# Kernel tuning notes

Measured on AMD Instinct MI355X. Metric: run time of the kernel, lower is better.

## Reference

```python
import jax, jax.numpy as jnp
import numpy as np

EMBED, HEADS, LEVELS, POINTS = 256, 8, 4, 4
HD = EMBED // HEADS
BS, NQ = 2, 16384
SHAPES = [(128, 128), (64, 64), (32, 32), (16, 16)]  # (H, W) per level
NV = sum(h * w for h, w in SHAPES)
EPS = 1e-5


def layernorm(x, g, b):
    mu = jnp.mean(x, -1, keepdims=True)
    var = jnp.mean((x - mu) ** 2, -1, keepdims=True)
    return (x - mu) / jnp.sqrt(var + EPS) * g + b


def bilinear_sample(vl, loc, H, W):
    # vl: (bs, heads, H*W, hd); loc: (bs, nq, heads, P, 2) normalized [0,1]
    # grid_sample semantics: align_corners=False, zero padding
    x = loc[..., 0] * W - 0.5
    y = loc[..., 1] * H - 0.5
    x0 = jnp.floor(x)
    y0 = jnp.floor(y)
    lx, ly = x - x0, y - y0
    x0 = x0.astype(jnp.int32)
    y0 = y0.astype(jnp.int32)
    gather = jax.vmap(jax.vmap(lambda t, i: t[i]))  # over (bs, heads)
    acc = None
    for dx, dy, w in ((0, 0, (1 - lx) * (1 - ly)), (1, 0, lx * (1 - ly)),
                      (0, 1, (1 - lx) * ly), (1, 1, lx * ly)):
        xi, yi = x0 + dx, y0 + dy
        valid = ((xi >= 0) & (xi < W) & (yi >= 0) & (yi < H)).astype(vl.dtype)
        idx = jnp.clip(yi, 0, H - 1) * W + jnp.clip(xi, 0, W - 1)
        idx = idx.transpose(0, 2, 1, 3)           # (bs, heads, nq, P)
        g = gather(vl, idx)                       # (bs, heads, nq, P, hd)
        wv = (w * valid).transpose(0, 2, 1, 3)[..., None]
        acc = g * wv if acc is None else acc + g * wv
    return acc


def forward(lidar_feat, feat_flatten, ref_2d, spatial_shapes, level_start_index,
            q_pose, W_off, b_off, W_attn, b_attn, W_val, b_val, W_out, b_out,
            ln1_g, ln1_b, ffn_w1, ffn_w2, ln2_g, ln2_b):
    identity = lidar_feat                         # (nq, bs, C)
    q = (lidar_feat + q_pose).transpose(1, 0, 2)  # (bs, nq, C)
    bs, nq, C = q.shape
    v = feat_flatten.transpose(1, 0, 2) @ W_val + b_val
    v = v.reshape(bs, -1, HEADS, HD)
    off = (q @ W_off + b_off).reshape(bs, nq, HEADS, LEVELS, POINTS, 2)
    aw = (q @ W_attn + b_attn).reshape(bs, nq, HEADS, LEVELS * POINTS)
    aw = jax.nn.softmax(aw, -1).reshape(bs, nq, HEADS, LEVELS, POINTS)
    ss = np.asarray(spatial_shapes)               # static level shapes
    lsi = np.asarray(level_start_index)
    norm = jnp.asarray(ss[:, ::-1].copy(), q.dtype)  # (L, 2) [W, H]
    loc = ref_2d[:, :, None, :, None, :] + off / norm[None, None, None, :, None, :]
    out = jnp.zeros((bs, nq, HEADS, HD), q.dtype)
    for l in range(LEVELS):
        H, W = int(ss[l, 0]), int(ss[l, 1])
        s = int(lsi[l])
        vl = v[:, s:s + H * W].transpose(0, 2, 1, 3)   # (bs, heads, HW, hd)
        sampled = bilinear_sample(vl, loc[:, :, :, l], H, W)
        out = out + jnp.einsum('bhqpd,bqhp->bqhd', sampled, aw[:, :, :, l, :])
    out = out.reshape(bs, nq, C) @ W_out + b_out
    out = out.transpose(1, 0, 2) + identity       # residual (dropout=eval noop)
    x = layernorm(out, ln1_g, ln1_b)
    x = layernorm(jnp.maximum(x @ ffn_w1, 0.0) @ ffn_w2 + x, ln2_g, ln2_b)
    return x


def setup_inputs():
    key = jax.random.key(0)
    ks = jax.random.split(key, 16)
    starts = np.cumsum([0] + [h * w for h, w in SHAPES])[:-1]
    d = {
        'lidar_feat': jax.random.normal(ks[0], (NQ, BS, EMBED), jnp.float32),
        'feat_flatten': jax.random.normal(ks[1], (NV, BS, EMBED), jnp.float32),
        'ref_2d': jax.random.uniform(ks[2], (BS, NQ, LEVELS, 2), jnp.float32),
        'spatial_shapes': jnp.array(SHAPES, jnp.int32),
        'level_start_index': jnp.array(starts, jnp.int32),
        'q_pose': jax.random.normal(ks[3], (NQ, BS, EMBED), jnp.float32),
        'W_off': 0.02 * jax.random.normal(ks[4], (EMBED, HEADS * LEVELS * POINTS * 2), jnp.float32),
        'b_off': 2.0 * jax.random.normal(ks[5], (HEADS * LEVELS * POINTS * 2,), jnp.float32),
        'W_attn': 0.02 * jax.random.normal(ks[6], (EMBED, HEADS * LEVELS * POINTS), jnp.float32),
        'b_attn': jnp.zeros((HEADS * LEVELS * POINTS,), jnp.float32),
        'W_val': 0.02 * jax.random.normal(ks[7], (EMBED, EMBED), jnp.float32),
        'b_val': jnp.zeros((EMBED,), jnp.float32),
        'W_out': 0.02 * jax.random.normal(ks[8], (EMBED, EMBED), jnp.float32),
        'b_out': jnp.zeros((EMBED,), jnp.float32),
        'ln1_g': jnp.ones((EMBED,), jnp.float32),
        'ln1_b': jnp.zeros((EMBED,), jnp.float32),
        'ffn_w1': 0.02 * jax.random.normal(ks[9], (EMBED, EMBED), jnp.float32),
        'ffn_w2': 0.02 * jax.random.normal(ks[10], (EMBED, EMBED), jnp.float32),
        'ln2_g': jnp.ones((EMBED,), jnp.float32),
        'ln2_b': jnp.zeros((EMBED,), jnp.float32),
    }
    return d


def reference(lidar_feat, feat_flatten, ref_2d, spatial_shapes, level_start_index,
              q_pose, W_off, b_off, W_attn, b_attn, W_val, b_val, W_out, b_out,
              ln1_g, ln1_b, ffn_w1, ffn_w2, ln2_g, ln2_b):
    return forward(lidar_feat, feat_flatten, ref_2d, spatial_shapes,
                   level_start_index, q_pose, W_off, b_off, W_attn, b_attn,
                   W_val, b_val, W_out, b_out, ln1_g, ln1_b, ffn_w1, ffn_w2,
                   ln2_g, ln2_b)
```

## Files before the change

### kernel.cpp

```cpp
#include <hip/hip_runtime.h>
#include <cstdint>

#define EMBED 256
#define HEADS 8
#define LEVELS 4
#define POINTS 4
#define BS 2
#define NQ 16384
#define NV 21760
#define MQ (BS*NQ)
#define MV (BS*NV)

typedef __attribute__((ext_vector_type(8))) short short8;
typedef __attribute__((ext_vector_type(4))) float f32x4;

__device__ __forceinline__ unsigned short f2bf(float f) {
    unsigned int u = __float_as_uint(f);
    u = (u + 0x7FFFu + ((u >> 16) & 1u)) >> 16;
    return (unsigned short)u;
}
__device__ __forceinline__ float bf2f(unsigned short h) {
    return __uint_as_float(((unsigned int)h) << 16);
}
__device__ __forceinline__ void glds16(const unsigned short* g, unsigned short* l) {
    __builtin_amdgcn_global_load_lds((const __attribute__((address_space(1))) void*)g,
                                     (__attribute__((address_space(3))) void*)l, 16, 0, 0);
}

struct WtArgs {
    const float* src[6];
    unsigned short* dst[6];
    int n[6];
};
__global__ __launch_bounds__(256) void prep_wt(WtArgs a)
{
    const int g = blockIdx.y;
    const int N = a.n[g];
    const int e = blockIdx.x * 256 + threadIdx.x;
    if (e >= 256 * N) return;
    const int k = e / N, n = e - k * N;
    a.dst[g][(size_t)n * 256 + k] = f2bf(a.src[g][e]);
}

template<int NCOLS, int STAGEF32, int LNF, int RELUF>
__global__ __launch_bounds__(512) void gemm_big(
    const unsigned short* __restrict__ A,
    const float* __restrict__ Af, const float* __restrict__ A2f, int inner,
    const unsigned short* __restrict__ Bt,
    const float* __restrict__ bias0, const float* __restrict__ bias1,
    const float* __restrict__ res,
    const float* __restrict__ lng, const float* __restrict__ lnb,
    float* __restrict__ outf, unsigned short* __restrict__ outh)
{
    constexpr int FN = NCOLS / 64;
    __shared__ unsigned short As[128 * 32];
    __shared__ unsigned short Bs[NCOLS * 32];
    __shared__ float2 sdLN[LNF ? 128 : 1][4];

    const int t = threadIdx.x, l = t & 63, w = t >> 6;
    const int wm = w >> 2, wn = w & 3;
    const int frow = l & 15, fgrp = l >> 4;
    const size_t brow = (size_t)blockIdx.x * 128;

    const int fslot = fgrp ^ ((frow & 3) ^ ((frow >> 2) & 3));
    const int srow = l >> 2;
    const int sswz = (l & 3) ^ ((srow & 3) ^ ((srow >> 2) & 3));
    const unsigned short* gB0 = Bt + ((size_t)(w * 16 + srow)) * 256 + sswz * 8;

    const unsigned short* gA = nullptr;
    const float* srcA = nullptr; const float* srcA2 = nullptr;
    int arow_s = 0, aslot_s = 0, aswz_s = 0;
    if constexpr (STAGEF32) {
        arow_s = t >> 2; aslot_s = t & 3;
        const int grow = (int)brow + arow_s;
        const int bidx = grow / inner, nn = grow - bidx * inner;
        srcA = Af + (size_t)(nn * BS + bidx) * 256;
        if (A2f) srcA2 = A2f + (size_t)(nn * BS + bidx) * 256;
        aswz_s = aslot_s ^ ((arow_s & 3) ^ ((arow_s >> 2) & 3));
    } else {
        gA = A + (brow + (size_t)(w * 16 + srow)) * 256 + sswz * 8;
    }

    f32x4 acc[4][FN];
#pragma unroll
    for (int i = 0; i < 4; ++i)
#pragma unroll
        for (int j = 0; j < FN; ++j) acc[i][j] = f32x4{0.f, 0.f, 0.f, 0.f};

    float4 pA0, pA1, pC0, pC1;
    if constexpr (STAGEF32) {
        pA0 = *(const float4*)(srcA + aslot_s * 8);
        pA1 = *(const float4*)(srcA + aslot_s * 8 + 4);
        if (srcA2) { pC0 = *(const float4*)(srcA2 + aslot_s * 8);
                     pC1 = *(const float4*)(srcA2 + aslot_s * 8 + 4); }
    }

    for (int k0 = 0; k0 < 256; k0 += 32) {
        glds16(gB0 + k0,         (unsigned short*)&Bs[w * 512]);
        glds16(gB0 + 32768 + k0, (unsigned short*)&Bs[(w + 8) * 512]);
        if constexpr (NCOLS == 384)
            glds16(gB0 + 65536 + k0, (unsigned short*)&Bs[(w + 16) * 512]);

        if constexpr (STAGEF32) {
            float c[8] = {pA0.x, pA0.y, pA0.z, pA0.w, pA1.x, pA1.y, pA1.z, pA1.w};
            if (srcA2) {
                c[0] += pC0.x; c[1] += pC0.y; c[2] += pC0.z; c[3] += pC0.w;
                c[4] += pC1.x; c[5] += pC1.y; c[6] += pC1.z; c[7] += pC1.w;
            }
            short8 pk;
#pragma unroll
            for (int i = 0; i < 8; ++i) pk[i] = (short)f2bf(c[i]);
            *reinterpret_cast<short8*>(&As[arow_s * 32 + aswz_s * 8]) = pk;
            if (k0 + 32 < 256) {
                pA0 = *(const float4*)(srcA + k0 + 32 + aslot_s * 8);
                pA1 = *(const float4*)(srcA + k0 + 32 + aslot_s * 8 + 4);
                if (srcA2) { pC0 = *(const float4*)(srcA2 + k0 + 32 + aslot_s * 8);
                             pC1 = *(const float4*)(srcA2 + k0 + 32 + aslot_s * 8 + 4); }
            }
        } else {
            glds16(gA + k0, (unsigned short*)&As[w * 512]);
        }
        __syncthreads();

        short8 af[4]; short8 bq[FN];
#pragma unroll
        for (int fm = 0; fm < 4; ++fm)
            af[fm] = *reinterpret_cast<const short8*>(&As[(wm * 64 + fm * 16 + frow) * 32 + fslot * 8]);
#pragma unroll
        for (int fn = 0; fn < FN; ++fn)
            bq[fn] = *reinterpret_cast<const short8*>(&Bs[(wn * (NCOLS / 4) + fn * 16 + frow) * 32 + fslot * 8]);
#pragma unroll
        for (int fm = 0; fm < 4; ++fm)
#pragma unroll
            for (int fn = 0; fn < FN; ++fn)
                acc[fm][fn] = __builtin_amdgcn_mfma_f32_16x16x32_bf16(af[fm], bq[fn], acc[fm][fn], 0, 0, 0);
        __syncthreads();
    }

    int cols[FN]; float bi[FN];
#pragma unroll
    for (int fn = 0; fn < FN; ++fn) {
        const int col = wn * (NCOLS / 4) + fn * 16 + frow;
        cols[fn] = col;
        float b = 0.f;
        if (bias0) {
            if (NCOLS == 384) b = (col < 256) ? bias0[col] : bias1[col - 256];
            else              b = bias0[col];
        }
        bi[fn] = b;
    }
#pragma unroll
    for (int fm = 0; fm < 4; ++fm)
#pragma unroll
        for (int j = 0; j < 4; ++j) {
            const size_t row = brow + wm * 64 + fm * 16 + fgrp * 4 + j;
#pragma unroll
            for (int fn = 0; fn < FN; ++fn) {
                float x = acc[fm][fn][j] + bi[fn];
                if (res)   x += res[row * NCOLS + cols[fn]];
                if (RELUF) x = fmaxf(x, 0.f);
                acc[fm][fn][j] = x;
            }
        }

    if constexpr (LNF) {
#pragma unroll
        for (int fm = 0; fm < 4; ++fm)
#pragma unroll
            for (int j = 0; j < 4; ++j) {
                float s1 = 0.f, s2 = 0.f;
#pragma unroll
                for (int fn = 0; fn < FN; ++fn) { const float x = acc[fm][fn][j]; s1 += x; s2 += x * x; }
#pragma unroll
                for (int o = 1; o < 16; o <<= 1) { s1 += __shfl_xor(s1, o); s2 += __shfl_xor(s2, o); }
                if (frow == 0)
                    sdLN[wm * 64 + fm * 16 + fgrp * 4 + j][wn] = make_float2(s1, s2);
            }
        __syncthreads();
        float gv[FN], bv[FN];
#pragma unroll
        for (int fn = 0; fn < FN; ++fn) { gv[fn] = lng[cols[fn]]; bv[fn] = lnb[cols[fn]]; }
#pragma unroll
        for (int fm = 0; fm < 4; ++fm)
#pragma unroll
            for (int j = 0; j < 4; ++j) {
                const int rl = wm * 64 + fm * 16 + fgrp * 4 + j;
                const float2 p0 = sdLN[rl][0], p1 = sdLN[rl][1], p2 = sdLN[rl][2], p3 = sdLN[rl][3];
                const float s1 = p0.x + p1.x + p2.x + p3.x;
                const float s2 = p0.y + p1.y + p2.y + p3.y;
                const float mu = s1 * (1.f / 256.f);
                const float var = s2 * (1.f / 256.f) - mu * mu;
                const float rstd = rsqrtf(var + 1e-5f);
                const size_t row = brow + rl;
#pragma unroll
                for (int fn = 0; fn < FN; ++fn) {
                    const float y = (acc[fm][fn][j] - mu) * rstd * gv[fn] + bv[fn];
                    if (outf) outf[row * NCOLS + cols[fn]] = y;
                    if (outh) outh[row * NCOLS + cols[fn]] = f2bf(y);
                }
            }
    } else {
#pragma unroll
        for (int fm = 0; fm < 4; ++fm)
#pragma unroll
            for (int j = 0; j < 4; ++j) {
                const size_t row = brow + wm * 64 + fm * 16 + fgrp * 4 + j;
#pragma unroll
                for (int fn = 0; fn < FN; ++fn) {
                    const float x = acc[fm][fn][j];
                    if (outf) outf[row * NCOLS + cols[fn]] = x;
                    if (outh) outh[row * NCOLS + cols[fn]] = f2bf(x);
                }
            }
    }
}

__global__ __launch_bounds__(512) void ffn_fused(
    const unsigned short* __restrict__ X,
    const unsigned short* __restrict__ W1t, const unsigned short* __restrict__ W2t,
    const float* __restrict__ lng, const float* __restrict__ lnb,
    float* __restrict__ outf)
{
    __shared__ unsigned short As[64 * 32];
    __shared__ unsigned short Bs[256 * 32];
    __shared__ unsigned short Hs[64 * 256];
    __shared__ float2 sdLN[64][4];

    const int t = threadIdx.x, l = t & 63, w = t >> 6;
    const int wm = w >> 2, wn = w & 3;
    const int frow = l & 15, fgrp = l >> 4;
    const size_t brow = (size_t)blockIdx.x * 64;

    const int fslot = fgrp ^ ((frow & 3) ^ ((frow >> 2) & 3));
    const int srow = l >> 2;
    const int sswz = (l & 3) ^ ((srow & 3) ^ ((srow >> 2) & 3));

    const unsigned short* gX  = X + (brow + (size_t)((w & 3) * 16 + srow)) * 256 + sswz * 8;
    const unsigned short* gW1 = W1t + ((size_t)(w * 16 + srow)) * 256 + sswz * 8;
    const unsigned short* gW2 = W2t + ((size_t)(w * 16 + srow)) * 256 + sswz * 8;

    f32x4 acc[2][4];

#pragma unroll
    for (int i = 0; i < 2; ++i)
#pragma unroll
        for (int j = 0; j < 4; ++j) acc[i][j] = f32x4{0.f, 0.f, 0.f, 0.f};

    for (int k0 = 0; k0 < 256; k0 += 32) {
        glds16(gW1 + k0,         (unsigned short*)&Bs[w * 512]);
        glds16(gW1 + 32768 + k0, (unsigned short*)&Bs[(w + 8) * 512]);
        if (w < 4) glds16(gX + k0, (unsigned short*)&As[w * 512]);
        __syncthreads();

        short8 af[2], bq[4];
#pragma unroll
        for (int fm = 0; fm < 2; ++fm)
            af[fm] = *reinterpret_cast<const short8*>(&As[(wm * 32 + fm * 16 + frow) * 32 + fslot * 8]);
#pragma unroll
        for (int fn = 0; fn < 4; ++fn)
            bq[fn] = *reinterpret_cast<const short8*>(&Bs[(wn * 64 + fn * 16 + frow) * 32 + fslot * 8]);
#pragma unroll
        for (int fm = 0; fm < 2; ++fm)
#pragma unroll
            for (int fn = 0; fn < 4; ++fn)
                acc[fm][fn] = __builtin_amdgcn_mfma_f32_16x16x32_bf16(af[fm], bq[fn], acc[fm][fn], 0, 0, 0);
        __syncthreads();
    }

#pragma unroll
    for (int fm = 0; fm < 2; ++fm)
#pragma unroll
        for (int fn = 0; fn < 4; ++fn) {
            const int col = wn * 64 + fn * 16 + frow;
#pragma unroll
            for (int j = 0; j < 4; ++j) {
                const int row = wm * 32 + fm * 16 + fgrp * 4 + j;
                const int ss = (col >> 3) ^ (row & 7);
                Hs[row * 256 + ss * 8 + (col & 7)] = f2bf(fmaxf(acc[fm][fn][j], 0.f));
            }
        }
    __syncthreads();

#pragma unroll
    for (int i = 0; i < 2; ++i)
#pragma unroll
        for (int j = 0; j < 4; ++j) acc[i][j] = f32x4{0.f, 0.f, 0.f, 0.f};

    for (int k0 = 0; k0 < 256; k0 += 32) {
        glds16(gW2 + k0,         (unsigned short*)&Bs[w * 512]);
        glds16(gW2 + 32768 + k0, (unsigned short*)&Bs[(w + 8) * 512]);
        __syncthreads();

        short8 af[2], bq[4];
#pragma unroll
        for (int fm = 0; fm < 2; ++fm) {
            const int row = wm * 32 + fm * 16 + frow;
            const int ksg = (k0 >> 3) + fgrp;
            const int ss = ksg ^ (row & 7);
            af[fm] = *reinterpret_cast<const short8*>(&Hs[row * 256 + ss * 8]);
        }
#pragma unroll
        for (int fn = 0; fn < 4; ++fn)
            bq[fn] = *reinterpret_cast<const short8*>(&Bs[(wn * 64 + fn * 16 + frow) * 32 + fslot * 8]);
#pragma unroll
        for (int fm = 0; fm < 2; ++fm)
#pragma unroll
            for (int fn = 0; fn < 4; ++fn)
                acc[fm][fn] = __builtin_amdgcn_mfma_f32_16x16x32_bf16(af[fm], bq[fn], acc[fm][fn], 0, 0, 0);
        __syncthreads();
    }

#pragma unroll
    for (int fm = 0; fm < 2; ++fm)
#pragma unroll
        for (int fn = 0; fn < 4; ++fn) {
            const int col = wn * 64 + fn * 16 + frow;
#pragma unroll
            for (int j = 0; j < 4; ++j) {
                const size_t row = brow + wm * 32 + fm * 16 + fgrp * 4 + j;
                acc[fm][fn][j] += bf2f(X[row * 256 + col]);
            }
        }
#pragma unroll
    for (int fm = 0; fm < 2; ++fm)
#pragma unroll
        for (int j = 0; j < 4; ++j) {
            float s1 = 0.f, s2 = 0.f;
#pragma unroll
            for (int fn = 0; fn < 4; ++fn) { const float x = acc[fm][fn][j]; s1 += x; s2 += x * x; }
#pragma unroll
            for (int o = 1; o < 16; o <<= 1) { s1 += __shfl_xor(s1, o); s2 += __shfl_xor(s2, o); }
            if (frow == 0)
                sdLN[wm * 32 + fm * 16 + fgrp * 4 + j][wn] = make_float2(s1, s2);
        }
    __syncthreads();
#pragma unroll
    for (int fm = 0; fm < 2; ++fm)
#pragma unroll
        for (int j = 0; j < 4; ++j) {
            const int rl = wm * 32 + fm * 16 + fgrp * 4 + j;
            const float2 p0 = sdLN[rl][0], p1 = sdLN[rl][1], p2 = sdLN[rl][2], p3 = sdLN[rl][3];
            const float s1 = p0.x + p1.x + p2.x + p3.x;
            const float s2 = p0.y + p1.y + p2.y + p3.y;
            const float mu = s1 * (1.f / 256.f);
            const float var = s2 * (1.f / 256.f) - mu * mu;
            const float rstd = rsqrtf(var + 1e-5f);
            const size_t row = brow + rl;
#pragma unroll
            for (int fn = 0; fn < 4; ++fn) {
                const int col = wn * 64 + fn * 16 + frow;
                outf[row * 256 + col] = (acc[fm][fn][j] - mu) * rstd * lng[col] + lnb[col];
            }
        }
}

#define LDDESC(dst, base)                         \
    _Pragma("unroll")                             \
    for (int j = 0; j < 16; ++j) dst[j] = dp[(base) + j];
#define LDRAW(dst, dsc)                           \
    _Pragma("unroll")                             \
    for (int j = 0; j < 16; ++j) dst[j] = *(const uint2*)(vd + dsc[j].y);
#define FMA16(dsc, raw)                           \
    _Pragma("unroll")                             \
    for (int j = 0; j < 16; ++j) {                \
        const float wgt = __uint_as_float(dsc[j].x);            \
        a0 += wgt * __uint_as_float(raw[j].x << 16);            \
        a1 += wgt * __uint_as_float(raw[j].x & 0xFFFF0000u);    \
        a2 += wgt * __uint_as_float(raw[j].y << 16);            \
        a3 += wgt * __uint_as_float(raw[j].y & 0xFFFF0000u);    \
    }

__global__ __launch_bounds__(256) void sampler_k(
    const unsigned short* __restrict__ oa,
    const float* __restrict__ ref2d,
    const unsigned short* __restrict__ v,
    unsigned short* __restrict__ outh)
{
    const int q0 = blockIdx.x * 4;
    const int t = threadIdx.x;

    __shared__ float s_off[4][256];
    __shared__ float s_aw[4][128];
    __shared__ float s_ref[4][8];
    __shared__ uint2 s_d[4][8][65];

    {
        const int tq = t >> 6, c = (t & 63) * 4;
        const ushort4 u = *(const ushort4*)(oa + (size_t)(q0 + tq) * 384 + c);
        s_off[tq][c + 0] = bf2f(u.x); s_off[tq][c + 1] = bf2f(u.y);
        s_off[tq][c + 2] = bf2f(u.z); s_off[tq][c + 3] = bf2f(u.w);
    }
    if (t < 128) {
        const int tq = t >> 5, c = (t & 31) * 4;
        const ushort4 u = *(const ushort4*)(oa + (size_t)(q0 + tq) * 384 + 256 + c);
        s_aw[tq][c + 0] = bf2f(u.x); s_aw[tq][c + 1] = bf2f(u.y);
        s_aw[tq][c + 2] = bf2f(u.z); s_aw[tq][c + 3] = bf2f(u.w);
    }
    if (t < 32) {
        const int tq = t >> 3;
        s_ref[tq][t & 7] = ref2d[(size_t)(q0 + tq) * 8 + (t & 7)];
    }
    __syncthreads();

    if (t < 32) {
        const int tq = t >> 3, h = t & 7;
        float* a = s_aw[tq] + h * 16;
        float m = -1e30f;
#pragma unroll
        for (int i = 0; i < 16; ++i) m = fmaxf(m, a[i]);
        float e[16], s = 0.f;
#pragma unroll
        for (int i = 0; i < 16; ++i) { e[i] = __expf(a[i] - m); s += e[i]; }
        const float inv = 1.f / s;
#pragma unroll
        for (int i = 0; i < 16; ++i) a[i] = e[i] * inv;
    }
    __syncthreads();

#pragma unroll
    for (int it = 0; it < 2; ++it) {
        const int item = t + it * 256;
        const int tq = item >> 7, hlp = item & 127;
        const int h = hlp >> 4, lp = hlp & 15, li = lp >> 2;
        const int Wl[4]  = {128, 64, 32, 16};
        const int S0l[4] = {0, 16384, 20480, 21504};
        const int Wi = Wl[li]; const float Wf = (float)Wi;
        const int b = (q0 + tq) >> 14;
        const float x = (s_ref[tq][li * 2 + 0] + s_off[tq][hlp * 2 + 0] / Wf) * Wf - 0.5f;
        const float y = (s_ref[tq][li * 2 + 1] + s_off[tq][hlp * 2 + 1] / Wf) * Wf - 0.5f;
        const float x0f = floorf(x), y0f = floorf(y);
        const float lx = x - x0f, ly = y - y0f;
        const int x0 = (int)x0f, y0 = (int)y0f;
        const float a = s_aw[tq][hlp];
        const float cw[4] = {(1.f - lx) * (1.f - ly) * a, lx * (1.f - ly) * a,
                             (1.f - lx) * ly * a,          lx * ly * a};
        const int base = b * NV + S0l[li];
#pragma unroll
        for (int c = 0; c < 4; ++c) {
            const int xi = x0 + (c & 1), yi = y0 + (c >> 1);
            const bool val = (xi >= 0) & (xi < Wi) & (yi >= 0) & (yi < Wi);
            const int xc = min(max(xi, 0), Wi - 1), yc = min(max(yi, 0), Wi - 1);
            const unsigned int ofs = (unsigned int)(base + yc * Wi + xc) * 256u + h * 32;
            s_d[tq][h][lp * 4 + c] = make_uint2(__float_as_uint(val ? cw[c] : 0.f), ofs);
        }
    }
    __syncthreads();

    const int tq = t >> 6, l = t & 63, h = l >> 3, dq = l & 7;
    const int rb = q0 + tq, b = rb >> 14, qi = rb & (NQ - 1);
    const unsigned short* vd = v + dq * 4;
    const uint2* dp = &s_d[tq][h][0];
    float a0 = 0.f, a1 = 0.f, a2 = 0.f, a3 = 0.f;

    uint2 dA[16], dB[16], rA[16], rB[16];
    LDDESC(dA, 0)
    LDRAW(rA, dA)
    LDDESC(dB, 16)
    LDRAW(rB, dB)
    FMA16(dA, rA)
    LDDESC(dA, 32)
    LDRAW(rA, dA)
    FMA16(dB, rB)
    LDDESC(dB, 48)
    LDRAW(rB, dB)
    FMA16(dA, rA)
    FMA16(dB, rB)

    ushort4 o; o.x = f2bf(a0); o.y = f2bf(a1); o.z = f2bf(a2); o.w = f2bf(a3);
    *(ushort4*)(outh + (size_t)(qi * BS + b) * 256 + h * 32 + dq * 4) = o;
}

extern "C" void kernel_launch(void* const* d_in, const int* in_sizes, int n_in,
                              void* d_out, int out_size, void* d_ws, size_t ws_size,
                              hipStream_t stream)
{
    const float* lidar  = (const float*)d_in[0];
    const float* feat   = (const float*)d_in[1];
    const float* ref2d  = (const float*)d_in[2];
    const float* q_pose = (const float*)d_in[5];
    const float* W_off  = (const float*)d_in[6];
    const float* b_off  = (const float*)d_in[7];
    const float* W_attn = (const float*)d_in[8];
    const float* b_attn = (const float*)d_in[9];
    const float* W_val  = (const float*)d_in[10];
    const float* b_val  = (const float*)d_in[11];
    const float* W_out  = (const float*)d_in[12];
    const float* b_out  = (const float*)d_in[13];
    const float* ln1_g  = (const float*)d_in[14];
    const float* ln1_b  = (const float*)d_in[15];
    const float* ffn_w1 = (const float*)d_in[16];
    const float* ffn_w2 = (const float*)d_in[17];
    const float* ln2_g  = (const float*)d_in[18];
    const float* ln2_b  = (const float*)d_in[19];

    float* out = (float*)d_out;
    char*  ws  = (char*)d_ws;

    unsigned short* vb   = (unsigned short*)(ws + 0);
    unsigned short* oa   = (unsigned short*)(ws + 22282240);
    unsigned short* smp  = (unsigned short*)(ws + 47448064);
    unsigned short* xln  = (unsigned short*)(ws + 64225280);
    unsigned short* wt   = (unsigned short*)(ws + 81002496);
    unsigned short* wt_val = wt;
    unsigned short* wt_oa  = wt + 65536;
    unsigned short* wt_out = wt + 163840;
    unsigned short* wt_f1  = wt + 229376;
    unsigned short* wt_f2  = wt + 294912;

    WtArgs wa;
    wa.src[0] = W_val;  wa.dst[0] = wt_val;          wa.n[0] = 256;
    wa.src[1] = W_off;  wa.dst[1] = wt_oa;           wa.n[1] = 256;
    wa.src[2] = W_attn; wa.dst[2] = wt_oa + 65536;   wa.n[2] = 128;
    wa.src[3] = W_out;  wa.dst[3] = wt_out;          wa.n[3] = 256;
    wa.src[4] = ffn_w1; wa.dst[4] = wt_f1;           wa.n[4] = 256;
    wa.src[5] = ffn_w2; wa.dst[5] = wt_f2;           wa.n[5] = 256;
    prep_wt<<<dim3(384, 6), dim3(256), 0, stream>>>(wa);

    gemm_big<256, 1, 0, 0><<<dim3(MV / 128), dim3(512), 0, stream>>>(
        nullptr, feat, nullptr, NV, wt_val, b_val, nullptr,
        nullptr, nullptr, nullptr, nullptr, vb);

    gemm_big<384, 1, 0, 0><<<dim3(MQ / 128), dim3(512), 0, stream>>>(
        nullptr, lidar, q_pose, NQ, wt_oa, b_off, b_attn,
        nullptr, nullptr, nullptr, nullptr, oa);

    sampler_k<<<dim3(MQ / 4), dim3(256), 0, stream>>>(oa, ref2d, vb, smp);

    gemm_big<256, 0, 1, 0><<<dim3(MQ / 128), dim3(512), 0, stream>>>(
        smp, nullptr, nullptr, 0, wt_out, b_out, nullptr,
        lidar, ln1_g, ln1_b, nullptr, xln);

    ffn_fused<<<dim3(MQ / 64), dim3(512), 0, stream>>>(
        xln, wt_f1, wt_f2, ln2_g, ln2_b, out);
}
```

Baseline: 204.5 us.

## Sort queries into spatial buckets and swizzle sampler blocks for L2 locality

Adds a counting sort (histogram, scan, scatter) that groups queries by their reference point in a 16x16 grid per batch. The sampler then reads queries through this permutation, and block IDs are remapped so that blocks on the same XCD-style stride handle contiguous sorted ranges. The aim is for neighbouring blocks to gather overlapping value-map rows and so improve cache hit rates. In exchange it adds four small kernel launches and atomics, and the sampler's reads of oa and its writes to smp become scattered.

```diff
diff --git a/kernel.cpp b/kernel.cpp
--- a/kernel.cpp
+++ b/kernel.cpp
@@ -10,6 +10,7 @@
 #define NV 21760
 #define MQ (BS*NQ)
 #define MV (BS*NV)
+#define NBKT 512
 
 typedef __attribute__((ext_vector_type(8))) short short8;
 typedef __attribute__((ext_vector_type(4))) float f32x4;
@@ -40,6 +41,49 @@
     if (e >= 256 * N) return;
     const int k = e / N, n = e - k * N;
     a.dst[g][(size_t)n * 256 + k] = f2bf(a.src[g][e]);
+}
+
+__global__ __launch_bounds__(512) void zero_k(int* __restrict__ hist)
+{
+    hist[threadIdx.x] = 0;
+}
+__global__ __launch_bounds__(256) void bucket_k(
+    const float* __restrict__ ref2d, int* __restrict__ bkt, int* __restrict__ hist)
+{
+    const int rb = blockIdx.x * 256 + threadIdx.x;
+    const float x = ref2d[(size_t)rb * 8 + 0];
+    const float y = ref2d[(size_t)rb * 8 + 1];
+    const int qx = min(15, max(0, (int)(x * 16.f)));
+    const int qy = min(15, max(0, (int)(y * 16.f)));
+    const int bv = (rb >> 14) * 256 + qy * 16 + qx;
+    bkt[rb] = bv;
+    atomicAdd(&hist[bv], 1);
+}
+__global__ __launch_bounds__(512) void scan_k(
+    const int* __restrict__ hist, int* __restrict__ offs)
+{
+    __shared__ int s[512];
+    const int t = threadIdx.x;
+    int v = hist[t];
+    s[t] = v;
+    __syncthreads();
+    int acc = v;
+#pragma unroll
+    for (int o = 1; o < 512; o <<= 1) {
+        int add = (t >= o) ? s[t - o] : 0;
+        __syncthreads();
+        acc += add;
+        s[t] = acc;
+        __syncthreads();
+    }
+    offs[t] = acc - v;
+}
+__global__ __launch_bounds__(256) void scatter_k(
+    const int* __restrict__ bkt, int* __restrict__ offs, int* __restrict__ perm)
+{
+    const int rb = blockIdx.x * 256 + threadIdx.x;
+    const int pos = atomicAdd(&offs[bkt[rb]], 1);
+    perm[pos] = rb;
 }
 
 template<int NCOLS, int STAGEF32, int LNF, int RELUF>
@@ -374,31 +418,38 @@
     const unsigned short* __restrict__ oa,
     const float* __restrict__ ref2d,
     const unsigned short* __restrict__ v,
+    const int* __restrict__ perm,
     unsigned short* __restrict__ outh)
 {
-    const int q0 = blockIdx.x * 4;
+    const int bid = blockIdx.x;
+    const int sbid = (bid & 7) * (MQ / 4 / 8) + (bid >> 3);
+    const int q0 = sbid * 4;
     const int t = threadIdx.x;
 
+    __shared__ int s_rb[4];
     __shared__ float s_off[4][256];
     __shared__ float s_aw[4][128];
     __shared__ float s_ref[4][8];
     __shared__ uint2 s_d[4][8][65];
 
+    if (t < 4) s_rb[t] = perm[q0 + t];
+    __syncthreads();
+
     {
         const int tq = t >> 6, c = (t & 63) * 4;
-        const ushort4 u = *(const ushort4*)(oa + (size_t)(q0 + tq) * 384 + c);
+        const ushort4 u = *(const ushort4*)(oa + (size_t)s_rb[tq] * 384 + c);
         s_off[tq][c + 0] = bf2f(u.x); s_off[tq][c + 1] = bf2f(u.y);
         s_off[tq][c + 2] = bf2f(u.z); s_off[tq][c + 3] = bf2f(u.w);
     }
     if (t < 128) {
         const int tq = t >> 5, c = (t & 31) * 4;
-        const ushort4 u = *(const ushort4*)(oa + (size_t)(q0 + tq) * 384 + 256 + c);
+        const ushort4 u = *(const ushort4*)(oa + (size_t)s_rb[tq] * 384 + 256 + c);
         s_aw[tq][c + 0] = bf2f(u.x); s_aw[tq][c + 1] = bf2f(u.y);
         s_aw[tq][c + 2] = bf2f(u.z); s_aw[tq][c + 3] = bf2f(u.w);
     }
     if (t < 32) {
         const int tq = t >> 3;
-        s_ref[tq][t & 7] = ref2d[(size_t)(q0 + tq) * 8 + (t & 7)];
+        s_ref[tq][t & 7] = ref2d[(size_t)s_rb[tq] * 8 + (t & 7)];
     }
     __syncthreads();
 
@@ -425,7 +476,7 @@
         const int Wl[4]  = {128, 64, 32, 16};
         const int S0l[4] = {0, 16384, 20480, 21504};
         const int Wi = Wl[li]; const float Wf = (float)Wi;
-        const int b = (q0 + tq) >> 14;
+        const int b = s_rb[tq] >> 14;
         const float x = (s_ref[tq][li * 2 + 0] + s_off[tq][hlp * 2 + 0] / Wf) * Wf - 0.5f;
         const float y = (s_ref[tq][li * 2 + 1] + s_off[tq][hlp * 2 + 1] / Wf) * Wf - 0.5f;
         const float x0f = floorf(x), y0f = floorf(y);
@@ -447,7 +498,7 @@
     __syncthreads();
 
     const int tq = t >> 6, l = t & 63, h = l >> 3, dq = l & 7;
-    const int rb = q0 + tq, b = rb >> 14, qi = rb & (NQ - 1);
+    const int rb = s_rb[tq], b = rb >> 14, qi = rb & (NQ - 1);
     const unsigned short* vd = v + dq * 4;
     const uint2* dp = &s_d[tq][h][0];
     float a0 = 0.f, a1 = 0.f, a2 = 0.f, a3 = 0.f;
@@ -501,6 +552,10 @@
     unsigned short* smp  = (unsigned short*)(ws + 47448064);
     unsigned short* xln  = (unsigned short*)(ws + 64225280);
     unsigned short* wt   = (unsigned short*)(ws + 81002496);
+    int* perm = (int*)(ws + 81788928);
+    int* bkt  = (int*)(ws + 81920000);
+    int* hist = (int*)(ws + 82051072);
+    int* offs = (int*)(ws + 82053120);
     unsigned short* wt_val = wt;
     unsigned short* wt_oa  = wt + 65536;
     unsigned short* wt_out = wt + 163840;
@@ -516,6 +571,11 @@
     wa.src[5] = ffn_w2; wa.dst[5] = wt_f2;           wa.n[5] = 256;
     prep_wt<<<dim3(384, 6), dim3(256), 0, stream>>>(wa);
 
+    zero_k<<<dim3(1), dim3(512), 0, stream>>>(hist);
+    bucket_k<<<dim3(MQ / 256), dim3(256), 0, stream>>>(ref2d, bkt, hist);
+    scan_k<<<dim3(1), dim3(512), 0, stream>>>(hist, offs);
+    scatter_k<<<dim3(MQ / 256), dim3(256), 0, stream>>>(bkt, offs, perm);
+
     gemm_big<256, 1, 0, 0><<<dim3(MV / 128), dim3(512), 0, stream>>>(
         nullptr, feat, nullptr, NV, wt_val, b_val, nullptr,
         nullptr, nullptr, nullptr, nullptr, vb);
@@ -524,7 +584,7 @@
         nullptr, lidar, q_pose, NQ, wt_oa, b_off, b_attn,
         nullptr, nullptr, nullptr, nullptr, oa);
 
-    sampler_k<<<dim3(MQ / 4), dim3(256), 0, stream>>>(oa, ref2d, vb, smp);
+    sampler_k<<<dim3(MQ / 4), dim3(256), 0, stream>>>(oa, ref2d, vb, perm, smp);
 
     gemm_big<256, 0, 1, 0><<<dim3(MQ / 128), dim3(512), 0, stream>>>(
         smp, nullptr, nullptr, 0, wt_out, b_out, nullptr,
```

Measured after the change: 212.0 us. +3.6%, slower.
